# Performance work log

Measured on AMD Instinct MI355X. Metric: run time of the kernel, lower is better.

Reference implementation:

```python
import jax, jax.numpy as jnp
import numpy as np

T, B, I, H, O = 512, 64, 1024, 1024, 1024

def setup_inputs() -> dict:
    key = jax.random.key(0)
    ks = jax.random.split(key, 6)
    return {
        'x': jax.random.normal(ks[0], (T, B, I), dtype=jnp.float32),
        'h0': jax.random.normal(ks[1], (B, H), dtype=jnp.float32),
        'w_i2h': jax.random.normal(ks[2], (H, I + H), dtype=jnp.float32) * (1.0 / np.sqrt(I + H)),
        'b_i2h': jax.random.normal(ks[3], (H,), dtype=jnp.float32) * 0.01,
        'w_h2o': jax.random.normal(ks[4], (O, H), dtype=jnp.float32) * (1.0 / np.sqrt(H)),
        'b_h2o': jax.random.normal(ks[5], (O,), dtype=jnp.float32) * 0.01,
    }

def reference(x, h0, w_i2h, b_i2h, w_h2o, b_h2o):
    # concat([x_t, h]) @ w_i2h.T  ==  x_t @ Wx.T + h @ Wh.T, with Wx = w_i2h[:, :I], Wh = w_i2h[:, I:]
    i_dim = x.shape[-1]
    wx = w_i2h[:, :i_dim]   # [H, I]
    wh = w_i2h[:, i_dim:]   # [H, H]
    # Batch the input projection over all timesteps (same math, efficient):
    xproj = jnp.einsum('tbi,hi->tbh', x, wx) + b_i2h  # [T, B, H]

    def step(h, xp):
        h_new = jnp.tanh(xp + h @ wh.T)      # [B, H]
        y_t = h_new @ w_h2o.T + b_h2o        # [B, O]
        return h_new, y_t

    _, ys = jax.lax.scan(step, h0, xproj)    # ys: [T, B, O]
    return ys
```

## Files before the change

### kernel.cpp

```cpp
#include <hip/hip_runtime.h>
#include <math.h>

typedef __attribute__((ext_vector_type(8))) short bf16x8;
typedef __attribute__((ext_vector_type(4))) int   i32x4;
typedef __attribute__((ext_vector_type(4))) float f32x4;
typedef __attribute__((ext_vector_type(4))) unsigned short u16x4;

__device__ __forceinline__ unsigned short f2bf(float x) {
  unsigned int u = __builtin_bit_cast(unsigned int, x);
  return (unsigned short)((u + 0x7fffu + ((u >> 16) & 1u)) >> 16);
}
__device__ __forceinline__ float bf2f(unsigned short h) {
  unsigned int u = ((unsigned int)h) << 16;
  return __builtin_bit_cast(float, u);
}
__device__ __forceinline__ float fast_tanh(float z) {
  float e;
  asm("v_exp_f32 %0, %1" : "=v"(e) : "v"(z * 2.8853900817779268f));
  return 1.0f - 2.0f * __builtin_amdgcn_rcpf(e + 1.0f);
}

__global__ void convert_kernel(const float* __restrict__ w_i2h,
                               const float* __restrict__ w_h2o,
                               const float* __restrict__ h0,
                               unsigned short* __restrict__ wx,
                               unsigned short* __restrict__ wh,
                               unsigned short* __restrict__ w2o,
                               unsigned short* __restrict__ hx,
                               int* __restrict__ flags) {
  int idx = blockIdx.x * 256 + threadIdx.x;
  if (idx < 4096) flags[idx] = 0;
  int e = idx * 4;
  const float* src;
  unsigned short* dst;
  if (e < 2097152) {
    int row = e >> 11, col = e & 2047;
    src = w_i2h + e;
    dst = (col < 1024) ? (wx + row * 1024 + col) : (wh + row * 1024 + (col - 1024));
  } else if (e < 3145728) {
    int i = e - 2097152; src = w_h2o + i; dst = w2o + i;
  } else {
    int i = e - 3145728; src = h0 + i; dst = hx + i;
  }
  float4 v = *(const float4*)src;
  u16x4 o = {f2bf(v.x), f2bf(v.y), f2bf(v.z), f2bf(v.w)};
  *(u16x4*)dst = o;
}

template <bool AF32, bool OUTBF16>
__global__ __launch_bounds__(256) void gemm_bt(const void* __restrict__ Ap,
                                               const unsigned short* __restrict__ B,
                                               const float* __restrict__ bias,
                                               void* __restrict__ Cp,
                                               int M, int N, int K) {
  __shared__ __attribute__((aligned(16))) unsigned short lA[128 * 64];
  __shared__ __attribute__((aligned(16))) unsigned short lB[128 * 64];
  const int tid = threadIdx.x;
  const int bx = blockIdx.x & 7;
  const int by = blockIdx.x >> 3;
  const int lane = tid & 63, w = tid >> 6;
  const int g = lane >> 4, l15 = lane & 15;
  const int wm = w >> 1, wn = w & 1;

  f32x4 acc[4][4];
#pragma unroll
  for (int i = 0; i < 4; ++i)
#pragma unroll
    for (int j = 0; j < 4; ++j) acc[i][j] = (f32x4){0.f, 0.f, 0.f, 0.f};

  const int nK = K >> 6;
  for (int kt = 0; kt < nK; ++kt) {
    const int k0 = kt << 6;
#pragma unroll
    for (int i = 0; i < 4; ++i) {
      int cl = i * 256 + tid;
      int row = cl >> 3, cc = cl & 7;
      bf16x8 av;
      if (AF32) {
        const float* ap = (const float*)Ap + (size_t)(by * 128 + row) * K + k0 + cc * 8;
        float4 f0 = *(const float4*)ap;
        float4 f1 = *(const float4*)(ap + 4);
        av = (bf16x8){(short)f2bf(f0.x), (short)f2bf(f0.y), (short)f2bf(f0.z), (short)f2bf(f0.w),
                      (short)f2bf(f1.x), (short)f2bf(f1.y), (short)f2bf(f1.z), (short)f2bf(f1.w)};
      } else {
        const unsigned short* ap = (const unsigned short*)Ap + (size_t)(by * 128 + row) * K + k0 + cc * 8;
        av = *(const bf16x8*)ap;
      }
      *(bf16x8*)&lA[(row * 8 + (cc ^ (row & 7))) * 8] = av;
      const unsigned short* bp = B + (size_t)(bx * 128 + row) * K + k0 + cc * 8;
      bf16x8 bv = *(const bf16x8*)bp;
      *(bf16x8*)&lB[(row * 8 + (cc ^ (row & 7))) * 8] = bv;
    }
    __syncthreads();
#pragma unroll
    for (int kk = 0; kk < 2; ++kk) {
      bf16x8 av[4], bv[4];
#pragma unroll
      for (int mt = 0; mt < 4; ++mt) {
        int r = wm * 64 + mt * 16 + l15;
        av[mt] = *(const bf16x8*)&lA[(r * 8 + ((kk * 4 + g) ^ (r & 7))) * 8];
      }
#pragma unroll
      for (int nt = 0; nt < 4; ++nt) {
        int r = wn * 64 + nt * 16 + l15;
        bv[nt] = *(const bf16x8*)&lB[(r * 8 + ((kk * 4 + g) ^ (r & 7))) * 8];
      }
#pragma unroll
      for (int mt = 0; mt < 4; ++mt)
#pragma unroll
        for (int nt = 0; nt < 4; ++nt)
          acc[mt][nt] = __builtin_amdgcn_mfma_f32_16x16x32_bf16(av[mt], bv[nt], acc[mt][nt], 0, 0, 0);
    }
    __syncthreads();
  }
#pragma unroll
  for (int mt = 0; mt < 4; ++mt) {
    int grow = by * 128 + wm * 64 + mt * 16 + g * 4;
#pragma unroll
    for (int nt = 0; nt < 4; ++nt) {
      int col = bx * 128 + wn * 64 + nt * 16 + l15;
      float bs = bias[col];
#pragma unroll
      for (int r = 0; r < 4; ++r) {
        size_t off = (size_t)(grow + r) * N + col;
        float v = acc[mt][nt][r] + bs;
        if (OUTBF16) ((unsigned short*)Cp)[off] = f2bf(v);
        else ((float*)Cp)[off] = v;
      }
    }
  }
}

#define SCAN_BLOCKS 256
__global__ __launch_bounds__(64, 1) void rnn_scan(const unsigned short* __restrict__ xproj,
                                                  const unsigned short* __restrict__ wh,
                                                  const unsigned short* __restrict__ w2o,
                                                  const float* __restrict__ b_h2o,
                                                  float* __restrict__ y,
                                                  unsigned short* __restrict__ hx,
                                                  int* __restrict__ flags) {
  const int tid = threadIdx.x;
  const int b = blockIdx.x;
  const int jt = b >> 2, bt = b & 3;
  const int g = tid >> 4, l15 = tid & 15;
  const int j0 = jt * 16, b0 = bt * 16;

  bf16x8 wb[32], wo[32];
#pragma unroll
  for (int kk = 0; kk < 32; ++kk) {
    wb[kk] = *(const bf16x8*)(wh  + (size_t)(j0 + l15) * 1024 + kk * 32 + g * 8);
    wo[kk] = *(const bf16x8*)(w2o + (size_t)(j0 + l15) * 1024 + kk * 32 + g * 8);
  }
  const float4 bias_o = *(const float4*)(b_h2o + j0 + g * 4);

  const int* fl = flags + (bt * 64 + tid) * 16;
  int* myflag = flags + (bt * 64 + jt) * 16;

  const int pofs = (b0 + l15) * 1024 + j0 + g * 4;

  for (int t = 0; t <= 512; ++t) {
    const unsigned short* hsrc = hx + (size_t)(t & 3) * 65536 + (size_t)b0 * 1024;

    uint2 xpc;
    if (t < 512)
      xpc = *(const uint2*)(xproj + (size_t)t * 65536 + pofs);

    int v;
    do {
      asm volatile("global_load_dword %0, %1, off sc0 sc1\n\ts_waitcnt vmcnt(0)"
                   : "=v"(v) : "v"(fl) : "memory");
    } while (__any(v < t));

    i32x4 ha[32];
#pragma unroll
    for (int kk = 0; kk < 32; ++kk) {
      const unsigned short* p = hsrc + (size_t)l15 * 1024 + kk * 32 + g * 8;
      asm volatile("global_load_dwordx4 %0, %1, off sc0 sc1"
                   : "=v"(ha[kk]) : "v"(p) : "memory");
    }

    if (t < 512) {
      unsigned short* hdst = hx + (size_t)((t + 1) & 3) * 65536;
      f32x4 acc[4];
#pragma unroll
      for (int i = 0; i < 4; ++i) acc[i] = (f32x4){0.f, 0.f, 0.f, 0.f};

#define MFMA_GROUP(base, n)                                                     \
      asm volatile("s_waitcnt vmcnt(" #n ")" ::: "memory");                     \
      __builtin_amdgcn_sched_barrier(0);                                        \
      _Pragma("unroll")                                                         \
      for (int kk = base; kk < base + 8; ++kk)                                  \
        acc[kk & 3] = __builtin_amdgcn_mfma_f32_16x16x32_bf16(                  \
            wb[kk], __builtin_bit_cast(bf16x8, ha[kk]), acc[kk & 3], 0, 0, 0);

      MFMA_GROUP(0, 24)
      MFMA_GROUP(8, 16)
      MFMA_GROUP(16, 8)
      MFMA_GROUP(24, 0)
#undef MFMA_GROUP

      f32x4 s = (acc[0] + acc[1]) + (acc[2] + acc[3]);

      {
        float z0 = s[0] + bf2f((unsigned short)(xpc.x & 0xFFFF));
        float z1 = s[1] + bf2f((unsigned short)(xpc.x >> 16));
        float z2 = s[2] + bf2f((unsigned short)(xpc.y & 0xFFFF));
        float z3 = s[3] + bf2f((unsigned short)(xpc.y >> 16));
        unsigned int v01 = (unsigned int)f2bf(fast_tanh(z0)) |
                           ((unsigned int)f2bf(fast_tanh(z1)) << 16);
        unsigned int v23 = (unsigned int)f2bf(fast_tanh(z2)) |
                           ((unsigned int)f2bf(fast_tanh(z3)) << 16);
        uint2 dvec = {v01, v23};
        unsigned short* p = hdst + pofs;
        asm volatile("global_store_dwordx2 %0, %1, off sc0 sc1"
                     :: "v"(p), "v"(dvec) : "memory");
      }

      f32x4 ay[4];
#pragma unroll
      for (int i = 0; i < 4; ++i) ay[i] = (f32x4){0.f, 0.f, 0.f, 0.f};
      if (t > 0) {
#pragma unroll
        for (int kk = 0; kk < 32; ++kk)
          ay[kk & 3] = __builtin_amdgcn_mfma_f32_16x16x32_bf16(
              wo[kk], __builtin_bit_cast(bf16x8, ha[kk]), ay[kk & 3], 0, 0, 0);
      }
      __builtin_amdgcn_sched_barrier(0);

      asm volatile("s_waitcnt vmcnt(0)" ::: "memory");
      if (tid == 0) {
        int tv = t + 1;
        asm volatile("global_store_dword %0, %1, off sc0 sc1"
                     :: "v"(myflag), "v"(tv) : "memory");
      }

      if (t > 0) {
        f32x4 sy = (ay[0] + ay[1]) + (ay[2] + ay[3]);
        sy[0] += bias_o.x; sy[1] += bias_o.y; sy[2] += bias_o.z; sy[3] += bias_o.w;
        *(f32x4*)(y + (size_t)(t - 1) * 65536 + pofs) = sy;
      }
    } else {
      asm volatile("s_waitcnt vmcnt(0)" ::: "memory");
      __builtin_amdgcn_sched_barrier(0);
      f32x4 ay[4];
#pragma unroll
      for (int i = 0; i < 4; ++i) ay[i] = (f32x4){0.f, 0.f, 0.f, 0.f};
#pragma unroll
      for (int kk = 0; kk < 32; ++kk)
        ay[kk & 3] = __builtin_amdgcn_mfma_f32_16x16x32_bf16(
            wo[kk], __builtin_bit_cast(bf16x8, ha[kk]), ay[kk & 3], 0, 0, 0);
      f32x4 sy = (ay[0] + ay[1]) + (ay[2] + ay[3]);
      sy[0] += bias_o.x; sy[1] += bias_o.y; sy[2] += bias_o.z; sy[3] += bias_o.w;
      *(f32x4*)(y + (size_t)(t - 1) * 65536 + pofs) = sy;
    }
  }
}

extern "C" void kernel_launch(void* const* d_in, const int* in_sizes, int n_in,
                              void* d_out, int out_size, void* d_ws, size_t ws_size,
                              hipStream_t stream) {
  const float* x     = (const float*)d_in[0];
  const float* h0    = (const float*)d_in[1];
  const float* w_i2h = (const float*)d_in[2];
  const float* b_i2h = (const float*)d_in[3];
  const float* w_h2o = (const float*)d_in[4];
  const float* b_h2o = (const float*)d_in[5];

  char* ws = (char*)d_ws;
  unsigned short* xproj = (unsigned short*)ws;
  unsigned short* hx    = (unsigned short*)(ws + 67108864);
  int*            flags = (int*)(ws + 67108864 + 524288);
  unsigned short* wx    = (unsigned short*)(ws + 67108864 + 524288 + 16384);
  unsigned short* wh    = wx + 1024 * 1024;
  unsigned short* w2o   = wh + 1024 * 1024;
  float* y = (float*)d_out;

  convert_kernel<<<3136, 256, 0, stream>>>(w_i2h, w_h2o, h0, wx, wh, w2o, hx, flags);

  gemm_bt<true, true><<<2048, 256, 0, stream>>>((const void*)x, wx, b_i2h,
                                                (void*)xproj, 32768, 1024, 1024);

  rnn_scan<<<SCAN_BLOCKS, 64, 0, stream>>>(xproj, wh, w2o, b_h2o, y, hx, flags);
}
```

Baseline: 1.476 ms.

## Replace flag-based step synchronization with tag bits embedded in hidden-state values

```diff
diff --git a/kernel.cpp b/kernel.cpp
--- a/kernel.cpp
+++ b/kernel.cpp
@@ -26,21 +26,32 @@
                                unsigned short* __restrict__ wx,
                                unsigned short* __restrict__ wh,
                                unsigned short* __restrict__ w2o,
-                               unsigned short* __restrict__ hx,
-                               int* __restrict__ flags) {
+                               unsigned short* __restrict__ hx) {
   int idx = blockIdx.x * 256 + threadIdx.x;
-  if (idx < 4096) flags[idx] = 0;
   int e = idx * 4;
+  if (e >= 3276800) return;
+  if (e >= 3211264) {
+    *(u16x4*)(hx + 65536 + (e - 3211264)) = (u16x4){3, 3, 3, 3};
+    return;
+  }
+  if (e >= 3145728) {
+    int i = e - 3145728;
+    float4 v = *(const float4*)(h0 + i);
+    u16x4 o = {f2bf(v.x), f2bf(v.y), f2bf(v.z), f2bf(v.w)};
+#pragma unroll
+    for (int k = 0; k < 4; ++k)
+      o[k] = (unsigned short)(((unsigned int)o[k] + 2u) & 0xFFFCu);
+    *(u16x4*)(hx + i) = o;
+    return;
+  }
   const float* src;
   unsigned short* dst;
   if (e < 2097152) {
     int row = e >> 11, col = e & 2047;
     src = w_i2h + e;
     dst = (col < 1024) ? (wx + row * 1024 + col) : (wh + row * 1024 + (col - 1024));
-  } else if (e < 3145728) {
+  } else {
     int i = e - 2097152; src = w_h2o + i; dst = w2o + i;
-  } else {
-    int i = e - 3145728; src = h0 + i; dst = hx + i;
   }
   float4 v = *(const float4*)src;
   u16x4 o = {f2bf(v.x), f2bf(v.y), f2bf(v.z), f2bf(v.w)};
@@ -137,8 +148,7 @@
                                                   const unsigned short* __restrict__ w2o,
                                                   const float* __restrict__ b_h2o,
                                                   float* __restrict__ y,
-                                                  unsigned short* __restrict__ hx,
-                                                  int* __restrict__ flags) {
+                                                  unsigned short* __restrict__ hx) {
   const int tid = threadIdx.x;
   const int b = blockIdx.x;
   const int jt = b >> 2, bt = b & 3;
@@ -153,65 +163,63 @@
   }
   const float4 bias_o = *(const float4*)(b_h2o + j0 + g * 4);
 
-  const int* fl = flags + (bt * 64 + tid) * 16;
-  int* myflag = flags + (bt * 64 + jt) * 16;
-
   const int pofs = (b0 + l15) * 1024 + j0 + g * 4;
+  const int cofs = (b0 + l15) * 1024 + g * 8;
 
   for (int t = 0; t <= 512; ++t) {
-    const unsigned short* hsrc = hx + (size_t)(t & 3) * 65536 + (size_t)b0 * 1024;
+    const unsigned short* src = hx + (size_t)(t & 1) * 65536;
+    const unsigned int pat2 = (unsigned int)((t >> 1) & 1) * 0x00010001u;
 
     uint2 xpc;
     if (t < 512)
       xpc = *(const uint2*)(xproj + (size_t)t * 65536 + pofs);
 
-    int v;
+    i32x4 c[32];
+    bool allok;
     do {
-      asm volatile("global_load_dword %0, %1, off sc0 sc1\n\ts_waitcnt vmcnt(0)"
-                   : "=v"(v) : "v"(fl) : "memory");
-    } while (__any(v < t));
-
-    i32x4 ha[32];
-#pragma unroll
-    for (int kk = 0; kk < 32; ++kk) {
-      const unsigned short* p = hsrc + (size_t)l15 * 1024 + kk * 32 + g * 8;
-      asm volatile("global_load_dwordx4 %0, %1, off sc0 sc1"
-                   : "=v"(ha[kk]) : "v"(p) : "memory");
-    }
+#pragma unroll
+      for (int kk = 0; kk < 32; ++kk) {
+        const unsigned short* p = src + cofs + kk * 32;
+        asm volatile("global_load_dwordx4 %0, %1, off sc0 sc1"
+                     : "=v"(c[kk]) : "v"(p) : "memory");
+      }
+      asm volatile("s_waitcnt vmcnt(0)" ::: "memory");
+      __builtin_amdgcn_sched_barrier(0);
+      unsigned int bad = 0;
+#pragma unroll
+      for (int kk = 0; kk < 32; ++kk) {
+        bad |= ((unsigned int)c[kk][0] ^ pat2) & 0x00030003u;
+        bad |= ((unsigned int)c[kk][1] ^ pat2) & 0x00030003u;
+        bad |= ((unsigned int)c[kk][2] ^ pat2) & 0x00030003u;
+        bad |= ((unsigned int)c[kk][3] ^ pat2) & 0x00030003u;
+      }
+      allok = (bad == 0);
+    } while (__any(!allok));
+    __builtin_amdgcn_sched_barrier(0);
 
     if (t < 512) {
-      unsigned short* hdst = hx + (size_t)((t + 1) & 3) * 65536;
+      unsigned short* dst = hx + (size_t)((t + 1) & 1) * 65536;
       f32x4 acc[4];
 #pragma unroll
       for (int i = 0; i < 4; ++i) acc[i] = (f32x4){0.f, 0.f, 0.f, 0.f};
-
-#define MFMA_GROUP(base, n)                                                     \
-      asm volatile("s_waitcnt vmcnt(" #n ")" ::: "memory");                     \
-      __builtin_amdgcn_sched_barrier(0);                                        \
-      _Pragma("unroll")                                                         \
-      for (int kk = base; kk < base + 8; ++kk)                                  \
-        acc[kk & 3] = __builtin_amdgcn_mfma_f32_16x16x32_bf16(                  \
-            wb[kk], __builtin_bit_cast(bf16x8, ha[kk]), acc[kk & 3], 0, 0, 0);
-
-      MFMA_GROUP(0, 24)
-      MFMA_GROUP(8, 16)
-      MFMA_GROUP(16, 8)
-      MFMA_GROUP(24, 0)
-#undef MFMA_GROUP
-
+#pragma unroll
+      for (int kk = 0; kk < 32; ++kk)
+        acc[kk & 3] = __builtin_amdgcn_mfma_f32_16x16x32_bf16(
+            wb[kk], __builtin_bit_cast(bf16x8, c[kk]), acc[kk & 3], 0, 0, 0);
       f32x4 s = (acc[0] + acc[1]) + (acc[2] + acc[3]);
 
+      const unsigned int tagn = (unsigned int)(((t + 1) >> 1) & 1);
       {
         float z0 = s[0] + bf2f((unsigned short)(xpc.x & 0xFFFF));
         float z1 = s[1] + bf2f((unsigned short)(xpc.x >> 16));
         float z2 = s[2] + bf2f((unsigned short)(xpc.y & 0xFFFF));
         float z3 = s[3] + bf2f((unsigned short)(xpc.y >> 16));
-        unsigned int v01 = (unsigned int)f2bf(fast_tanh(z0)) |
-                           ((unsigned int)f2bf(fast_tanh(z1)) << 16);
-        unsigned int v23 = (unsigned int)f2bf(fast_tanh(z2)) |
-                           ((unsigned int)f2bf(fast_tanh(z3)) << 16);
-        uint2 dvec = {v01, v23};
-        unsigned short* p = hdst + pofs;
+        unsigned int h0v = (((unsigned int)f2bf(fast_tanh(z0)) + 2u) & 0xFFFCu) | tagn;
+        unsigned int h1v = (((unsigned int)f2bf(fast_tanh(z1)) + 2u) & 0xFFFCu) | tagn;
+        unsigned int h2v = (((unsigned int)f2bf(fast_tanh(z2)) + 2u) & 0xFFFCu) | tagn;
+        unsigned int h3v = (((unsigned int)f2bf(fast_tanh(z3)) + 2u) & 0xFFFCu) | tagn;
+        uint2 dvec = {h0v | (h1v << 16), h2v | (h3v << 16)};
+        unsigned short* p = dst + pofs;
         asm volatile("global_store_dwordx2 %0, %1, off sc0 sc1"
                      :: "v"(p), "v"(dvec) : "memory");
       }
@@ -223,16 +231,10 @@
 #pragma unroll
         for (int kk = 0; kk < 32; ++kk)
           ay[kk & 3] = __builtin_amdgcn_mfma_f32_16x16x32_bf16(
-              wo[kk], __builtin_bit_cast(bf16x8, ha[kk]), ay[kk & 3], 0, 0, 0);
+              wo[kk], __builtin_bit_cast(bf16x8, c[kk]), ay[kk & 3], 0, 0, 0);
       }
       __builtin_amdgcn_sched_barrier(0);
-
       asm volatile("s_waitcnt vmcnt(0)" ::: "memory");
-      if (tid == 0) {
-        int tv = t + 1;
-        asm volatile("global_store_dword %0, %1, off sc0 sc1"
-                     :: "v"(myflag), "v"(tv) : "memory");
-      }
 
       if (t > 0) {
         f32x4 sy = (ay[0] + ay[1]) + (ay[2] + ay[3]);
@@ -240,15 +242,13 @@
         *(f32x4*)(y + (size_t)(t - 1) * 65536 + pofs) = sy;
       }
     } else {
-      asm volatile("s_waitcnt vmcnt(0)" ::: "memory");
-      __builtin_amdgcn_sched_barrier(0);
       f32x4 ay[4];
 #pragma unroll
       for (int i = 0; i < 4; ++i) ay[i] = (f32x4){0.f, 0.f, 0.f, 0.f};
 #pragma unroll
       for (int kk = 0; kk < 32; ++kk)
         ay[kk & 3] = __builtin_amdgcn_mfma_f32_16x16x32_bf16(
-            wo[kk], __builtin_bit_cast(bf16x8, ha[kk]), ay[kk & 3], 0, 0, 0);
+            wo[kk], __builtin_bit_cast(bf16x8, c[kk]), ay[kk & 3], 0, 0, 0);
       f32x4 sy = (ay[0] + ay[1]) + (ay[2] + ay[3]);
       sy[0] += bias_o.x; sy[1] += bias_o.y; sy[2] += bias_o.z; sy[3] += bias_o.w;
       *(f32x4*)(y + (size_t)(t - 1) * 65536 + pofs) = sy;
@@ -269,16 +269,15 @@
   char* ws = (char*)d_ws;
   unsigned short* xproj = (unsigned short*)ws;
   unsigned short* hx    = (unsigned short*)(ws + 67108864);
-  int*            flags = (int*)(ws + 67108864 + 524288);
-  unsigned short* wx    = (unsigned short*)(ws + 67108864 + 524288 + 16384);
+  unsigned short* wx    = (unsigned short*)(ws + 67108864 + 262144);
   unsigned short* wh    = wx + 1024 * 1024;
   unsigned short* w2o   = wh + 1024 * 1024;
   float* y = (float*)d_out;
 
-  convert_kernel<<<3136, 256, 0, stream>>>(w_i2h, w_h2o, h0, wx, wh, w2o, hx, flags);
+  convert_kernel<<<3200, 256, 0, stream>>>(w_i2h, w_h2o, h0, wx, wh, w2o, hx);
 
   gemm_bt<true, true><<<2048, 256, 0, stream>>>((const void*)x, wx, b_i2h,
                                                 (void*)xproj, 32768, 1024, 1024);
 
-  rnn_scan<<<SCAN_BLOCKS, 64, 0, stream>>>(xproj, wh, w2o, b_h2o, y, hx, flags);
-}
+  rnn_scan<<<SCAN_BLOCKS, 64, 0, stream>>>(xproj, wh, w2o, b_h2o, y, hx);
+}
```

Measured after the change: 3.562 ms. 141% more time.

## Fuse input-projection GEMM with RNN scan using producer-consumer readiness flags

Applied to the files above, without the earlier changes.

```diff
diff --git a/kernel.cpp b/kernel.cpp
--- a/kernel.cpp
+++ b/kernel.cpp
@@ -29,7 +29,7 @@
                                unsigned short* __restrict__ hx,
                                int* __restrict__ flags) {
   int idx = blockIdx.x * 256 + threadIdx.x;
-  if (idx < 4096) flags[idx] = 0;
+  if (idx < 4352) flags[idx] = 0;
   int e = idx * 4;
   const float* src;
   unsigned short* dst;
@@ -47,99 +47,103 @@
   *(u16x4*)dst = o;
 }
 
-template <bool AF32, bool OUTBF16>
-__global__ __launch_bounds__(256) void gemm_bt(const void* __restrict__ Ap,
-                                               const unsigned short* __restrict__ B,
-                                               const float* __restrict__ bias,
-                                               void* __restrict__ Cp,
-                                               int M, int N, int K) {
+#define TOTAL_BLOCKS 512
+__global__ __launch_bounds__(256, 2) void fused_kernel(const float* __restrict__ x,
+                                                       const float* __restrict__ b_i2h,
+                                                       const unsigned short* __restrict__ wx,
+                                                       const unsigned short* __restrict__ wh,
+                                                       const unsigned short* __restrict__ w2o,
+                                                       const float* __restrict__ b_h2o,
+                                                       unsigned short* __restrict__ xproj,
+                                                       float* __restrict__ y,
+                                                       unsigned short* __restrict__ hx,
+                                                       int* __restrict__ flags,
+                                                       int* __restrict__ xready) {
   __shared__ __attribute__((aligned(16))) unsigned short lA[128 * 64];
   __shared__ __attribute__((aligned(16))) unsigned short lB[128 * 64];
+
+  if (blockIdx.x >= 256) {
+    const int wkr = blockIdx.x - 256;
+    const int bx = wkr & 7, byg = wkr >> 3;
+    const int tid = threadIdx.x;
+    const int lane = tid & 63, w = tid >> 6;
+    const int g = lane >> 4, l15 = lane & 15;
+    const int wm = w >> 1, wn = w & 1;
+    const int K = 1024;
+
+    for (int i = 0; i < 8; ++i) {
+      const int by = byg + 32 * i;
+      f32x4 acc[4][4];
+#pragma unroll
+      for (int a = 0; a < 4; ++a)
+#pragma unroll
+        for (int c = 0; c < 4; ++c) acc[a][c] = (f32x4){0.f, 0.f, 0.f, 0.f};
+
+      for (int kt = 0; kt < 16; ++kt) {
+        const int k0 = kt << 6;
+#pragma unroll
+        for (int s = 0; s < 4; ++s) {
+          int cl = s * 256 + tid;
+          int row = cl >> 3, cc = cl & 7;
+          const float* ap = x + (size_t)(by * 128 + row) * K + k0 + cc * 8;
+          float4 f0 = *(const float4*)ap;
+          float4 f1 = *(const float4*)(ap + 4);
+          bf16x8 av = (bf16x8){(short)f2bf(f0.x), (short)f2bf(f0.y), (short)f2bf(f0.z), (short)f2bf(f0.w),
+                               (short)f2bf(f1.x), (short)f2bf(f1.y), (short)f2bf(f1.z), (short)f2bf(f1.w)};
+          *(bf16x8*)&lA[(row * 8 + (cc ^ (row & 7))) * 8] = av;
+          const unsigned short* bp = wx + (size_t)(bx * 128 + row) * K + k0 + cc * 8;
+          bf16x8 bv = *(const bf16x8*)bp;
+          *(bf16x8*)&lB[(row * 8 + (cc ^ (row & 7))) * 8] = bv;
+        }
+        __syncthreads();
+#pragma unroll
+        for (int kk = 0; kk < 2; ++kk) {
+          bf16x8 av[4], bv[4];
+#pragma unroll
+          for (int mt = 0; mt < 4; ++mt) {
+            int r = wm * 64 + mt * 16 + l15;
+            av[mt] = *(const bf16x8*)&lA[(r * 8 + ((kk * 4 + g) ^ (r & 7))) * 8];
+          }
+#pragma unroll
+          for (int nt = 0; nt < 4; ++nt) {
+            int r = wn * 64 + nt * 16 + l15;
+            bv[nt] = *(const bf16x8*)&lB[(r * 8 + ((kk * 4 + g) ^ (r & 7))) * 8];
+          }
+#pragma unroll
+          for (int mt = 0; mt < 4; ++mt)
+#pragma unroll
+            for (int nt = 0; nt < 4; ++nt)
+              acc[mt][nt] = __builtin_amdgcn_mfma_f32_16x16x32_bf16(av[mt], bv[nt], acc[mt][nt], 0, 0, 0);
+        }
+        __syncthreads();
+      }
+#pragma unroll
+      for (int mt = 0; mt < 4; ++mt) {
+        int grow = by * 128 + wm * 64 + mt * 16 + g * 4;
+#pragma unroll
+        for (int nt = 0; nt < 4; ++nt) {
+          int col = bx * 128 + wn * 64 + nt * 16 + l15;
+          float bs = b_i2h[col];
+#pragma unroll
+          for (int r = 0; r < 4; ++r) {
+            unsigned int hv = f2bf(acc[mt][nt][r] + bs);
+            const unsigned short* p = xproj + (size_t)(grow + r) * 1024 + col;
+            asm volatile("global_store_short %0, %1, off sc0 sc1"
+                         :: "v"(p), "v"(hv) : "memory");
+          }
+        }
+      }
+      asm volatile("s_waitcnt vmcnt(0)" ::: "memory");
+      __syncthreads();
+      if (tid == 0)
+        __hip_atomic_fetch_add(xready + by, 1, __ATOMIC_RELAXED, __HIP_MEMORY_SCOPE_AGENT);
+      __syncthreads();
+    }
+    return;
+  }
+
   const int tid = threadIdx.x;
-  const int bx = blockIdx.x & 7;
-  const int by = blockIdx.x >> 3;
-  const int lane = tid & 63, w = tid >> 6;
-  const int g = lane >> 4, l15 = lane & 15;
-  const int wm = w >> 1, wn = w & 1;
-
-  f32x4 acc[4][4];
-#pragma unroll
-  for (int i = 0; i < 4; ++i)
-#pragma unroll
-    for (int j = 0; j < 4; ++j) acc[i][j] = (f32x4){0.f, 0.f, 0.f, 0.f};
-
-  const int nK = K >> 6;
-  for (int kt = 0; kt < nK; ++kt) {
-    const int k0 = kt << 6;
-#pragma unroll
-    for (int i = 0; i < 4; ++i) {
-      int cl = i * 256 + tid;
-      int row = cl >> 3, cc = cl & 7;
-      bf16x8 av;
-      if (AF32) {
-        const float* ap = (const float*)Ap + (size_t)(by * 128 + row) * K + k0 + cc * 8;
-        float4 f0 = *(const float4*)ap;
-        float4 f1 = *(const float4*)(ap + 4);
-        av = (bf16x8){(short)f2bf(f0.x), (short)f2bf(f0.y), (short)f2bf(f0.z), (short)f2bf(f0.w),
-                      (short)f2bf(f1.x), (short)f2bf(f1.y), (short)f2bf(f1.z), (short)f2bf(f1.w)};
-      } else {
-        const unsigned short* ap = (const unsigned short*)Ap + (size_t)(by * 128 + row) * K + k0 + cc * 8;
-        av = *(const bf16x8*)ap;
-      }
-      *(bf16x8*)&lA[(row * 8 + (cc ^ (row & 7))) * 8] = av;
-      const unsigned short* bp = B + (size_t)(bx * 128 + row) * K + k0 + cc * 8;
-      bf16x8 bv = *(const bf16x8*)bp;
-      *(bf16x8*)&lB[(row * 8 + (cc ^ (row & 7))) * 8] = bv;
-    }
-    __syncthreads();
-#pragma unroll
-    for (int kk = 0; kk < 2; ++kk) {
-      bf16x8 av[4], bv[4];
-#pragma unroll
-      for (int mt = 0; mt < 4; ++mt) {
-        int r = wm * 64 + mt * 16 + l15;
-        av[mt] = *(const bf16x8*)&lA[(r * 8 + ((kk * 4 + g) ^ (r & 7))) * 8];
-      }
-#pragma unroll
-      for (int nt = 0; nt < 4; ++nt) {
-        int r = wn * 64 + nt * 16 + l15;
-        bv[nt] = *(const bf16x8*)&lB[(r * 8 + ((kk * 4 + g) ^ (r & 7))) * 8];
-      }
-#pragma unroll
-      for (int mt = 0; mt < 4; ++mt)
-#pragma unroll
-        for (int nt = 0; nt < 4; ++nt)
-          acc[mt][nt] = __builtin_amdgcn_mfma_f32_16x16x32_bf16(av[mt], bv[nt], acc[mt][nt], 0, 0, 0);
-    }
-    __syncthreads();
-  }
-#pragma unroll
-  for (int mt = 0; mt < 4; ++mt) {
-    int grow = by * 128 + wm * 64 + mt * 16 + g * 4;
-#pragma unroll
-    for (int nt = 0; nt < 4; ++nt) {
-      int col = bx * 128 + wn * 64 + nt * 16 + l15;
-      float bs = bias[col];
-#pragma unroll
-      for (int r = 0; r < 4; ++r) {
-        size_t off = (size_t)(grow + r) * N + col;
-        float v = acc[mt][nt][r] + bs;
-        if (OUTBF16) ((unsigned short*)Cp)[off] = f2bf(v);
-        else ((float*)Cp)[off] = v;
-      }
-    }
-  }
-}
-
-#define SCAN_BLOCKS 256
-__global__ __launch_bounds__(64, 1) void rnn_scan(const unsigned short* __restrict__ xproj,
-                                                  const unsigned short* __restrict__ wh,
-                                                  const unsigned short* __restrict__ w2o,
-                                                  const float* __restrict__ b_h2o,
-                                                  float* __restrict__ y,
-                                                  unsigned short* __restrict__ hx,
-                                                  int* __restrict__ flags) {
-  const int tid = threadIdx.x;
+  if (tid >= 64) return;
   const int b = blockIdx.x;
   const int jt = b >> 2, bt = b & 3;
   const int g = tid >> 4, l15 = tid & 15;
@@ -155,15 +159,29 @@
 
   const int* fl = flags + (bt * 64 + tid) * 16;
   int* myflag = flags + (bt * 64 + jt) * 16;
-
   const int pofs = (b0 + l15) * 1024 + j0 + g * 4;
+
+  int xconf = -1;
 
   for (int t = 0; t <= 512; ++t) {
     const unsigned short* hsrc = hx + (size_t)(t & 3) * 65536 + (size_t)b0 * 1024;
 
     uint2 xpc;
-    if (t < 512)
-      xpc = *(const uint2*)(xproj + (size_t)t * 65536 + pofs);
+    if (t < 512) {
+      int byg = t >> 1;
+      if (byg > xconf) {
+        const int* xr = xready + (byg & ~3);
+        i32x4 rv;
+        do {
+          asm volatile("global_load_dwordx4 %0, %1, off sc0 sc1\n\ts_waitcnt vmcnt(0)"
+                       : "=v"(rv) : "v"(xr) : "memory");
+        } while (rv[0] < 8 || rv[1] < 8 || rv[2] < 8 || rv[3] < 8);
+        xconf = (byg & ~3) + 3;
+      }
+      const unsigned short* xp = xproj + (size_t)t * 65536 + pofs;
+      asm volatile("global_load_dwordx2 %0, %1, off sc0 sc1"
+                   : "=v"(xpc) : "v"(xp) : "memory");
+    }
 
     int v;
     do {
@@ -270,15 +288,14 @@
   unsigned short* xproj = (unsigned short*)ws;
   unsigned short* hx    = (unsigned short*)(ws + 67108864);
   int*            flags = (int*)(ws + 67108864 + 524288);
-  unsigned short* wx    = (unsigned short*)(ws + 67108864 + 524288 + 16384);
+  int*            xready = flags + 4096;
+  unsigned short* wx    = (unsigned short*)(ws + 67108864 + 524288 + 17408);
   unsigned short* wh    = wx + 1024 * 1024;
   unsigned short* w2o   = wh + 1024 * 1024;
   float* y = (float*)d_out;
 
   convert_kernel<<<3136, 256, 0, stream>>>(w_i2h, w_h2o, h0, wx, wh, w2o, hx, flags);
 
-  gemm_bt<true, true><<<2048, 256, 0, stream>>>((const void*)x, wx, b_i2h,
-                                                (void*)xproj, 32768, 1024, 1024);
-
-  rnn_scan<<<SCAN_BLOCKS, 64, 0, stream>>>(xproj, wh, w2o, b_h2o, y, hx, flags);
-}
+  fused_kernel<<<TOTAL_BLOCKS, 256, 0, stream>>>(x, b_i2h, wx, wh, w2o, b_h2o,
+                                                 xproj, y, hx, flags, xready);
+}
```

After: 3.342 ms. +126.5%, slower.
